# Optimization experiments

Measured on AMD Instinct MI355X. Metric: run time of the kernel, lower is better.

Reference implementation:

```python
import jax, jax.numpy as jnp
import numpy as np

N = 50000      # nodes
E = 800000     # edges (avg degree 16)
C = 16         # hidden states per generative model
M = 32         # discrete symbol alphabet size
G = 8          # n_gen


def setup_inputs() -> dict:
    key = jax.random.key(0)
    k = jax.random.split(key, 6)
    u = lambda kk, shp: jax.random.uniform(kk, shp, jnp.float32, -5.0, 5.0)
    return {
        "x": jax.random.randint(k[0], (N,), 0, M),
        "edge_index": jax.random.randint(k[1], (2, E), 0, N),
        "B0": u(k[2], (C, M, G)),       # CGMMLayer_0.B
        "Pi": u(k[3], (C, G)),          # CGMMLayer_0.Pi
        "B1": u(k[4], (C, M, G)),       # CGMMLayer.B
        "Q_neigh": u(k[5], (C, C, G)),  # CGMMLayer.Q_neigh
    }


def reference(x, edge_index, B0, Pi, B1, Q_neigh):
    n = x.shape[0]
    # ---- layer 0 (CGMMLayer_0) ----
    sm_B0 = jax.nn.softmax(B0, axis=1)   # [C,M,G], softmax over symbols
    sm_Pi = jax.nn.softmax(Pi, axis=0)   # [C,G],   softmax over states
    # unnorm_posterior = Pi * B[:, x]    -> [N,C,G]
    unnorm0 = sm_Pi[None, :, :] * jnp.transpose(sm_B0[:, x, :], (1, 0, 2))
    norm0 = unnorm0.sum(1, keepdims=True)           # [N,1,G]
    ll0 = jnp.log(norm0[:, 0, :])                   # [N,G]
    post0 = unnorm0 / norm0                         # [N,C,G] = h_prev
    # ---- layer 1 (CGMMLayer) ----
    sm_Q = jax.nn.softmax(Q_neigh, axis=0)          # [C,C,G], softmax over dim 0
    sm_B1 = jax.nn.softmax(B1, axis=1)              # [C,M,G]
    src, dst = edge_index[0], edge_index[1]
    gathered = post0[dst]                           # [E,C,G] edge gather
    aggr_sum = jax.ops.segment_sum(gathered, src, num_segments=n)   # [N,C,G]
    cnt = jax.ops.segment_sum(jnp.ones((src.shape[0],), jnp.float32), src, num_segments=n)
    aggr = aggr_sum / jnp.maximum(cnt, 1.0)[:, None, None]          # scatter-mean
    B_nodes = jnp.transpose(sm_B1[:, x, :], (1, 0, 2))[:, :, None, :]  # [N,C,1,G]
    # joint over (current state i, neighbor state l): [N,C,C,G]
    unnorm1 = B_nodes * sm_Q[None, :, :, :] * aggr[:, None, :, :]
    norm1 = unnorm1.sum((1, 2), keepdims=True)      # [N,1,1,G]
    post1 = (unnorm1 / norm1).sum(2)                # [N,C,G] posterior_i
    ll1 = jnp.log(norm1[:, 0, 0, :])                # [N,G]
    log_likelihood = jnp.stack([ll0, ll1], axis=1)  # [N,2,G] (per layer)
    return log_likelihood, post1
```

## Files before the change

kernel.cpp:

```cpp
#include <hip/hip_runtime.h>
#include <hip/hip_bf16.h>
#include <math.h>

#define Nn 50000
#define Ee 800000
#define Cc 16
#define Mm 32
#define Gg 8

#define P1B 250
#define NBK 1024
#define BSZ 49
#define SEGE 20
#define SEGW 21

__device__ __forceinline__ float ldin(const void* p, int idx, int isbf) {
    if (isbf) return __bfloat162float(((const __hip_bfloat16*)p)[idx]);
    return ((const float*)p)[idx];
}
__device__ __forceinline__ void stout(void* p, size_t idx, float v, int isbf) {
    if (isbf) ((__hip_bfloat16*)p)[idx] = __float2bfloat16(v);
    else ((float*)p)[idx] = v;
}
__device__ __forceinline__ unsigned short f2bf(float f) {
    unsigned u = __float_as_uint(f);
    return (unsigned short)((u + 0x7FFFu + ((u >> 16) & 1u)) >> 16);
}
__device__ __forceinline__ float bflo(unsigned v) { return __uint_as_float(v << 16); }

__device__ __forceinline__ int detect_bf16(const void* B0, int tid, int* sflag) {
    if (tid < 64) {
        unsigned wv = ((const unsigned*)B0)[tid];
        unsigned ex = (wv >> 7) & 0xFFu;
        unsigned long long m = __ballot(ex >= 120u && ex <= 130u);
        if (tid == 0) *sflag = (__popcll(m) >= 48) ? 1 : 0;
    }
    __syncthreads();
    return *sflag;
}

__device__ __forceinline__ void sm_col(float* a, int base, int stride, int cnt) {
    float mx = -1e30f;
    for (int k = 0; k < cnt; ++k) mx = fmaxf(mx, a[base + k * stride]);
    float s = 0.f;
    for (int k = 0; k < cnt; ++k) {
        float e = __expf(a[base + k * stride] - mx);
        a[base + k * stride] = e;
        s += e;
    }
    float inv = 1.0f / s;
    for (int k = 0; k < cnt; ++k) a[base + k * stride] *= inv;
}

__global__ __launch_bounds__(512) void bucket_tables(
        const int* __restrict__ ei,
        const int* __restrict__ x,
        const void* __restrict__ B0,
        const void* __restrict__ Pi,
        const void* __restrict__ B1,
        const void* __restrict__ Q,
        unsigned* __restrict__ segbuf,
        float* __restrict__ lntabws,
        float* __restrict__ smB1ws,
        float* __restrict__ QRws,
        int* __restrict__ flag_ws) {
    int b = blockIdx.x, tid = threadIdx.x;
    __shared__ unsigned shb[NBK + NBK * SEGE];
    __shared__ int sflag;

    if (b < P1B) {
        int* scnt = (int*)shb;
        unsigned* sstage = shb + NBK;
        for (int i = tid; i < NBK; i += 512) scnt[i] = 0;
        __syncthreads();
        const int4* ei4 = (const int4*)ei;
        const int qbase = b * 800;
        for (int q = tid; q < 800; q += 512) {
            int4 sv = ei4[qbase + q];
            int4 dv = ei4[200000 + qbase + q];
            int ds_[4] = { dv.x, dv.y, dv.z, dv.w };
            int xs_[4];
#pragma unroll
            for (int k = 0; k < 4; ++k) xs_[k] = x[ds_[k]];
#pragma unroll
            for (int k = 0; k < 4; ++k) {
                int s = (k == 0) ? sv.x : (k == 1) ? sv.y : (k == 2) ? sv.z : sv.w;
                int bk = s / BSZ;
                int pos = atomicAdd(&scnt[bk], 1);
                if (pos < SEGE)
                    sstage[bk * SEGE + pos] =
                        ((unsigned)(s - bk * BSZ) << 5) | (unsigned)xs_[k];
            }
        }
        __syncthreads();
        for (int idx = tid; idx < NBK * SEGW; idx += 512) {
            int bk = idx / SEGW;
            int j  = idx - bk * SEGW;
            int c  = scnt[bk]; c = c < SEGE ? c : SEGE;
            unsigned v = (j == 0) ? (unsigned)c : sstage[bk * SEGE + (j - 1)];
            segbuf[((size_t)bk * P1B + b) * SEGW + j] = v;
        }
        return;
    }

    float* sh = (float*)shb;
    const int isbf = detect_bf16(B0, tid, &sflag);
    if (tid == 0) flag_ws[0] = isbf;
    for (int i = tid; i < Cc * Mm * Gg; i += 512) sh[i] = ldin(B1, i, isbf);
    __syncthreads();
    if (tid < 128) sm_col(sh, (tid >> 3) * (Mm * Gg) + (tid & 7), Gg, Mm);
    __syncthreads();
    for (int i = tid; i < Cc * Mm * Gg; i += 512) smB1ws[i] = sh[i];
    __syncthreads();
    for (int i = tid; i < Cc * Cc * Gg; i += 512) sh[i] = ldin(Q, i, isbf);
    __syncthreads();
    if (tid < 128) sm_col(sh, (tid >> 3) * Gg + (tid & 7), Cc * Gg, Cc);
    __syncthreads();
    float* sQg = sh + 4608;
    for (int t = tid; t < Cc * Cc * Gg; t += 512) {
        int i = t >> 7, rem = t & 127, l = rem >> 3, g = rem & 7;
        sQg[g * 256 + i * 16 + l] = sh[t];
    }
    __syncthreads();
    float* sB0 = sh;
    float* sPi = sh + 4096;
    float* sInv = sh + 4224;
    for (int i = tid; i < Cc * Mm * Gg; i += 512) sB0[i] = ldin(B0, i, isbf);
    if (tid < Cc * Gg) sPi[tid] = ldin(Pi, tid, isbf);
    __syncthreads();
    if (tid < 128) {
        sm_col(sB0, (tid >> 3) * (Mm * Gg) + (tid & 7), Gg, Mm);
    } else if (tid < 128 + Gg) {
        sm_col(sPi, tid - 128, Gg, Cc);
    }
    __syncthreads();
    if (tid < Mm * Gg) {
        int mm = tid >> 3, g = tid & 7;
        float s = 0.f;
#pragma unroll
        for (int c = 0; c < Cc; ++c) s += sPi[c * Gg + g] * sB0[c * (Mm * Gg) + mm * Gg + g];
        lntabws[tid] = logf(s);
        sInv[tid] = 1.0f / s;
    }
    __syncthreads();
    float* sRf = sh + 6656;
    for (int t = tid; t < 4096; t += 512) {
        int m = t >> 7, rem = t & 127, l = rem >> 3, g = rem & 7;
        float pv = sPi[l * 8 + g] * sB0[l * (Mm * Gg) + m * 8 + g] * sInv[m * 8 + g];
        sRf[t] = bflo((unsigned)f2bf(pv));
    }
    __syncthreads();
    for (int t = tid; t < 4096; t += 512) {
        int m = t >> 7, rem = t & 127, i = rem >> 3, g = rem & 7;
        float s = 0.f;
#pragma unroll
        for (int l = 0; l < 16; ++l) s += sQg[g * 256 + i * 16 + l] * sRf[m * 128 + l * 8 + g];
        QRws[t] = s;
    }
}

__global__ __launch_bounds__(512) void place_aggr(
        const unsigned* __restrict__ segbuf,
        const int* __restrict__ x,
        const float* __restrict__ smB1ws,
        const float* __restrict__ QRws,
        const float* __restrict__ lntabws,
        const int* __restrict__ flag_ws,
        void* __restrict__ out) {
    __shared__ float sQR[32 * 144];
    __shared__ float lnt[256];
    __shared__ int hist[BSZ * 32];
    __shared__ int scl[256];
    int b = blockIdx.x, tid = threadIdx.x;
    const int isbf = flag_ws[0];
    const unsigned* strip = segbuf + (size_t)b * (P1B * SEGW);

    for (int t = tid; t < 4096; t += 512) {
        int m = t >> 7, rem = t & 127, i = rem >> 3, g = rem & 7;
        sQR[m * 144 + i * 9 + g] = QRws[t];
    }
    for (int t = tid; t < 256; t += 512) lnt[t] = lntabws[t];
    for (int t = tid; t < BSZ * 32; t += 512) hist[t] = 0;
    if (tid < P1B) scl[tid] = (int)strip[tid * SEGW];
    __syncthreads();

    {
        for (int w = tid; w < P1B * SEGW; w += 512) {
            unsigned pk = strip[w];
            int seg = w / SEGW;
            int j   = w - seg * SEGW;
            if (j >= 1 && j <= scl[seg])
                atomicAdd(&hist[pk], 1);
        }
    }
    __syncthreads();

    const int nbase = b * BSZ;
    int limt = Nn - nbase; if (limt > BSZ) limt = BSZ; if (limt < 0) limt = 0;

    for (int t = tid; t < limt * 8; t += 512) {
        int n = t >> 3, g = t & 7;
        stout(out, (size_t)(nbase + n) * (2 * Gg) + g, lnt[x[nbase + n] * 8 + g], isbf);
    }

    const int lane = tid & 63, wib = tid >> 6;
    const int ii = lane >> 3, gW = lane & 7;
    const int i0 = 2 * ii, i1 = i0 + 1;
    const float* q0 = sQR + i0 * 9 + gW;
    const float* q1 = q0 + 9;

    for (int n = wib; n < limt; n += 8) {
        const int* hp = hist + n * 32;
        int xvn = x[nbase + n];
        float b0c = smB1ws[i0 * (Mm * Gg) + xvn * Gg + gW];
        float b1c = smB1ws[i1 * (Mm * Gg) + xvn * Gg + gW];
        float qa0 = 0.f, qa1 = 0.f;
        int d = 0;
#pragma unroll
        for (int mm = 0; mm < 8; ++mm) {
            int4 hv = ((const int4*)hp)[mm];
            int m4 = mm * 4;
            d += hv.x + hv.y + hv.z + hv.w;
            qa0 += (float)hv.x * q0[(m4 + 0) * 144] + (float)hv.y * q0[(m4 + 1) * 144]
                 + (float)hv.z * q0[(m4 + 2) * 144] + (float)hv.w * q0[(m4 + 3) * 144];
            qa1 += (float)hv.x * q1[(m4 + 0) * 144] + (float)hv.y * q1[(m4 + 1) * 144]
                 + (float)hv.z * q1[(m4 + 2) * 144] + (float)hv.w * q1[(m4 + 3) * 144];
        }
        float invd = 1.0f / fmaxf((float)d, 1.0f);
        qa0 *= invd; qa1 *= invd;
        float v0 = b0c * qa0, v1 = b1c * qa1;
        float nrm = v0 + v1;
        nrm += __shfl_xor(nrm, 8, 64);
        nrm += __shfl_xor(nrm, 16, 64);
        nrm += __shfl_xor(nrm, 32, 64);
        float invn = 1.0f / nrm;
        int ng = nbase + n;
        size_t pbase = (size_t)Nn * 2 * Gg + (size_t)ng * (Cc * Gg);
        stout(out, pbase + i0 * Gg + gW, v0 * invn, isbf);
        stout(out, pbase + i1 * Gg + gW, v1 * invn, isbf);
        if (ii == 0) stout(out, (size_t)ng * (2 * Gg) + Gg + gW, logf(nrm), isbf);
    }
}

extern "C" void kernel_launch(void* const* d_in, const int* in_sizes, int n_in,
                              void* d_out, int out_size, void* d_ws, size_t ws_size,
                              hipStream_t stream) {
    const int* x  = (const int*)d_in[0];
    const int* ei = (const int*)d_in[1];
    const void* B0 = d_in[2];
    const void* Pi = d_in[3];
    const void* B1 = d_in[4];
    const void* Q  = d_in[5];

    float* ws = (float*)d_ws;
    int*   flag    = (int*)ws;
    float* smB1ws  = ws + 128;
    float* lntabws = smB1ws + 4096;
    float* QRws    = lntabws + 256;
    unsigned* segbuf = (unsigned*)(QRws + 4096);

    bucket_tables<<<P1B + 1, 512, 0, stream>>>(
        ei, x, B0, Pi, B1, Q, segbuf, lntabws, smB1ws, QRws, flag);

    place_aggr<<<NBK, 512, 0, stream>>>(
        segbuf, x, smB1ws, QRws, lntabws, flag, d_out);
}
```

Baseline: 121.4 us.

## Pack bucket entries into 16-bit halves and widen bucketing blocks to 1024 threads

Each staged edge record (local node index and symbol) is stored as a 16-bit value, and two are packed per 32-bit word, which roughly halves the segment buffer written by the bucketing kernel and read by the aggregation kernel. The bucketing kernel now runs 1024 threads per block, so each thread handles one int4 of edges and writes one bucket's cell directly instead of looping. The consumer reads only the words that are valid in each segment, using two threads per segment. This cuts global traffic and loop overhead, at the cost of per-thread serial write loops and uneven work per thread.

```diff
diff --git a/kernel.cpp b/kernel.cpp
--- a/kernel.cpp
+++ b/kernel.cpp
@@ -12,7 +12,7 @@
 #define NBK 1024
 #define BSZ 49
 #define SEGE 20
-#define SEGW 21
+#define SEGW 11
 
 __device__ __forceinline__ float ldin(const void* p, int idx, int isbf) {
     if (isbf) return __bfloat162float(((const __hip_bfloat16*)p)[idx]);
@@ -52,7 +52,7 @@
     for (int k = 0; k < cnt; ++k) a[base + k * stride] *= inv;
 }
 
-__global__ __launch_bounds__(512) void bucket_tables(
+__global__ __launch_bounds__(1024) void bucket_tables(
         const int* __restrict__ ei,
         const int* __restrict__ x,
         const void* __restrict__ B0,
@@ -65,19 +65,20 @@
         float* __restrict__ QRws,
         int* __restrict__ flag_ws) {
     int b = blockIdx.x, tid = threadIdx.x;
-    __shared__ unsigned shb[NBK + NBK * SEGE];
+    __shared__ unsigned shb[11264];
     __shared__ int sflag;
 
     if (b < P1B) {
         int* scnt = (int*)shb;
-        unsigned* sstage = shb + NBK;
-        for (int i = tid; i < NBK; i += 512) scnt[i] = 0;
+        unsigned short* sstage = (unsigned short*)(shb + 1024);
+        scnt[tid] = 0;
         __syncthreads();
         const int4* ei4 = (const int4*)ei;
         const int qbase = b * 800;
-        for (int q = tid; q < 800; q += 512) {
-            int4 sv = ei4[qbase + q];
-            int4 dv = ei4[200000 + qbase + q];
+        if (tid < 800) {
+            int q = qbase + tid;
+            int4 sv = ei4[q];
+            int4 dv = ei4[200000 + q];
             int ds_[4] = { dv.x, dv.y, dv.z, dv.w };
             int xs_[4];
 #pragma unroll
@@ -89,16 +90,18 @@
                 int pos = atomicAdd(&scnt[bk], 1);
                 if (pos < SEGE)
                     sstage[bk * SEGE + pos] =
-                        ((unsigned)(s - bk * BSZ) << 5) | (unsigned)xs_[k];
+                        (unsigned short)(((s - bk * BSZ) << 5) | xs_[k]);
             }
         }
         __syncthreads();
-        for (int idx = tid; idx < NBK * SEGW; idx += 512) {
-            int bk = idx / SEGW;
-            int j  = idx - bk * SEGW;
-            int c  = scnt[bk]; c = c < SEGE ? c : SEGE;
-            unsigned v = (j == 0) ? (unsigned)c : sstage[bk * SEGE + (j - 1)];
-            segbuf[((size_t)bk * P1B + b) * SEGW + j] = v;
+        {
+            int c = scnt[tid]; c = c < SEGE ? c : SEGE;
+            unsigned* cell = segbuf + ((size_t)tid * P1B + b) * SEGW;
+            cell[0] = (unsigned)c;
+            const unsigned short* st = sstage + tid * SEGE;
+            int nw = (c + 1) >> 1;
+            for (int w = 0; w < nw; ++w)
+                cell[1 + w] = (unsigned)st[2 * w] | ((unsigned)st[2 * w + 1] << 16);
         }
         return;
     }
@@ -106,18 +109,18 @@
     float* sh = (float*)shb;
     const int isbf = detect_bf16(B0, tid, &sflag);
     if (tid == 0) flag_ws[0] = isbf;
-    for (int i = tid; i < Cc * Mm * Gg; i += 512) sh[i] = ldin(B1, i, isbf);
+    for (int i = tid; i < Cc * Mm * Gg; i += 1024) sh[i] = ldin(B1, i, isbf);
     __syncthreads();
     if (tid < 128) sm_col(sh, (tid >> 3) * (Mm * Gg) + (tid & 7), Gg, Mm);
     __syncthreads();
-    for (int i = tid; i < Cc * Mm * Gg; i += 512) smB1ws[i] = sh[i];
-    __syncthreads();
-    for (int i = tid; i < Cc * Cc * Gg; i += 512) sh[i] = ldin(Q, i, isbf);
+    for (int i = tid; i < Cc * Mm * Gg; i += 1024) smB1ws[i] = sh[i];
+    __syncthreads();
+    for (int i = tid; i < Cc * Cc * Gg; i += 1024) sh[i] = ldin(Q, i, isbf);
     __syncthreads();
     if (tid < 128) sm_col(sh, (tid >> 3) * Gg + (tid & 7), Cc * Gg, Cc);
     __syncthreads();
     float* sQg = sh + 4608;
-    for (int t = tid; t < Cc * Cc * Gg; t += 512) {
+    for (int t = tid; t < Cc * Cc * Gg; t += 1024) {
         int i = t >> 7, rem = t & 127, l = rem >> 3, g = rem & 7;
         sQg[g * 256 + i * 16 + l] = sh[t];
     }
@@ -125,7 +128,7 @@
     float* sB0 = sh;
     float* sPi = sh + 4096;
     float* sInv = sh + 4224;
-    for (int i = tid; i < Cc * Mm * Gg; i += 512) sB0[i] = ldin(B0, i, isbf);
+    for (int i = tid; i < Cc * Mm * Gg; i += 1024) sB0[i] = ldin(B0, i, isbf);
     if (tid < Cc * Gg) sPi[tid] = ldin(Pi, tid, isbf);
     __syncthreads();
     if (tid < 128) {
@@ -144,13 +147,13 @@
     }
     __syncthreads();
     float* sRf = sh + 6656;
-    for (int t = tid; t < 4096; t += 512) {
+    for (int t = tid; t < 4096; t += 1024) {
         int m = t >> 7, rem = t & 127, l = rem >> 3, g = rem & 7;
         float pv = sPi[l * 8 + g] * sB0[l * (Mm * Gg) + m * 8 + g] * sInv[m * 8 + g];
         sRf[t] = bflo((unsigned)f2bf(pv));
     }
     __syncthreads();
-    for (int t = tid; t < 4096; t += 512) {
+    for (int t = tid; t < 4096; t += 1024) {
         int m = t >> 7, rem = t & 127, i = rem >> 3, g = rem & 7;
         float s = 0.f;
 #pragma unroll
@@ -185,12 +188,17 @@
     __syncthreads();
 
     {
-        for (int w = tid; w < P1B * SEGW; w += 512) {
-            unsigned pk = strip[w];
-            int seg = w / SEGW;
-            int j   = w - seg * SEGW;
-            if (j >= 1 && j <= scl[seg])
-                atomicAdd(&hist[pk], 1);
+        if (tid < 2 * P1B) {
+            int seg = tid >> 1, par = tid & 1;
+            int c = scl[seg];
+            int nw = (c + 1) >> 1;
+            const unsigned* sp = strip + seg * SEGW + 1;
+            for (int w = par; w < nw; w += 2) {
+                unsigned pk = sp[w];
+                atomicAdd(&hist[pk & 0x7ffu], 1);
+                int e2 = 2 * w + 1;
+                if (e2 < c) atomicAdd(&hist[(pk >> 16) & 0x7ffu], 1);
+            }
         }
     }
     __syncthreads();
@@ -259,7 +267,7 @@
     float* QRws    = lntabws + 256;
     unsigned* segbuf = (unsigned*)(QRws + 4096);
 
-    bucket_tables<<<P1B + 1, 512, 0, stream>>>(
+    bucket_tables<<<P1B + 1, 1024, 0, stream>>>(
         ei, x, B0, Pi, B1, Q, segbuf, lntabws, smB1ws, QRws, flag);
 
     place_aggr<<<NBK, 512, 0, stream>>>(
```

New measurement: 112.4 us. 1.08x faster.
